# Kernel optimization log

Measured on AMD Instinct MI355X. Metric: run time of the kernel, lower is better.

## Reference

```python
import jax, jax.numpy as jnp
import numpy as np

C1 = 512  # channels1 (query input dim)
C = 512   # channels (model dim)


def setup_inputs() -> dict:
    key = jax.random.key(0)
    ks = jax.random.split(key, 12)
    B, Lq, Lk = 8, 2048, 2048
    s1 = 1.0 / np.sqrt(C1)
    s = 1.0 / np.sqrt(C)
    return {
        "rep": jax.random.normal(ks[0], (B, Lq, C1), dtype=jnp.float32),
        "rep1": jax.random.normal(ks[1], (B, Lk, C), dtype=jnp.float32),
        "Wq_w": jax.random.uniform(ks[2], (C1, C), jnp.float32, -s1, s1),
        "Wq_b": jax.random.uniform(ks[3], (C,), jnp.float32, -s1, s1),
        "Wk_w": jax.random.uniform(ks[4], (C, C), jnp.float32, -s, s),
        "Wk_b": jax.random.uniform(ks[5], (C,), jnp.float32, -s, s),
        "Wv_w": jax.random.uniform(ks[6], (C, C), jnp.float32, -s, s),
        "Wv_b": jax.random.uniform(ks[7], (C,), jnp.float32, -s, s),
        "FC_w": jax.random.uniform(ks[8], (C, C), jnp.float32, -s, s),
        "FC_b": jax.random.uniform(ks[9], (C,), jnp.float32, -s, s),
    }


def reference(rep, rep1, Wq_w, Wq_b, Wk_w, Wk_b, Wv_w, Wv_b, FC_w, FC_b):
    # Linear + ReLU projections (single head)
    q = jax.nn.relu(jnp.einsum('blc,cd->bld', rep, Wq_w) + Wq_b)    # [B,Lq,C]
    k = jax.nn.relu(jnp.einsum('blc,cd->bld', rep1, Wk_w) + Wk_b)   # [B,Lk,C]
    v = jax.nn.relu(jnp.einsum('blc,cd->bld', rep1, Wv_w) + Wv_b)   # [B,Lk,C]
    scores = jnp.einsum('bqd,bkd->bqk', q, k) / jnp.sqrt(jnp.float32(C))
    attn = jax.nn.softmax(scores, axis=-1)                           # [B,Lq,Lk]
    out = jnp.einsum('bqk,bkd->bqd', attn, v)                        # [B,Lq,C]
    out = jax.nn.relu(jnp.einsum('bld,de->ble', out, FC_w) + FC_b)
    return out
```

## Files before the change

kernel.cpp:

```cpp
#include <hip/hip_runtime.h>


typedef __attribute__((ext_vector_type(8))) short short8;
typedef __attribute__((ext_vector_type(4))) float f32x4;

#define SEQ 2048
#define CH 512
#define NB 8
#define MTOT (NB * SEQ)

#define GLDS16(gp, lp)                                                                  \
  __builtin_amdgcn_global_load_lds((const __attribute__((address_space(1))) void*)(gp), \
                                   (__attribute__((address_space(3))) void*)(lp), 16, 0, 0)

__device__ __forceinline__ unsigned short f2bf(float f) {
  unsigned u = __float_as_uint(f);
  u += 0x7fffu + ((u >> 16) & 1u);
  return (unsigned short)(u >> 16);
}

__global__ void cvt_bf16_kernel(const float* __restrict__ in0, unsigned short* __restrict__ out0,
                                const float* __restrict__ in1, unsigned short* __restrict__ out1) {
  int blk = blockIdx.x;
  const float* in = (blk < 4096) ? in0 : in1;
  unsigned short* out = (blk < 4096) ? out0 : out1;
  blk &= 4095;
  long i = ((long)blk * 256 + threadIdx.x) * 8;
  float4 a = *(const float4*)(in + i);
  float4 b = *(const float4*)(in + i + 4);
  ushort4 o0, o1;
  o0.x = f2bf(a.x); o0.y = f2bf(a.y); o0.z = f2bf(a.z); o0.w = f2bf(a.w);
  o1.x = f2bf(b.x); o1.y = f2bf(b.y); o1.z = f2bf(b.z); o1.w = f2bf(b.w);
  *(ushort4*)(out + i) = o0;
  *(ushort4*)(out + i + 4) = o1;
}

__global__ __launch_bounds__(256) void wtrans_kernel(const float* __restrict__ W0,
                                                     const float* __restrict__ W1,
                                                     const float* __restrict__ W2,
                                                     const float* __restrict__ W3,
                                                     unsigned short* __restrict__ Wt) {
  __shared__ __attribute__((aligned(16))) unsigned short tile[64 * 72];
  const int z = blockIdx.z;
  const float* W = (z == 0) ? W0 : (z == 1) ? W1 : (z == 2) ? W2 : W3;
  unsigned short* Wtz = Wt + (long)z * 512 * 512;
  const int t = threadIdx.x;
  const int k0 = blockIdx.y * 64, n0 = blockIdx.x * 64;
  const int r = t >> 4, cq = (t & 15) * 4;
#pragma unroll
  for (int j = 0; j < 4; ++j) {
    int row = r + 16 * j;
    float4 v = *(const float4*)&W[(long)(k0 + row) * 512 + n0 + cq];
    tile[row * 72 + cq + 0] = f2bf(v.x);
    tile[row * 72 + cq + 1] = f2bf(v.y);
    tile[row * 72 + cq + 2] = f2bf(v.z);
    tile[row * 72 + cq + 3] = f2bf(v.w);
  }
  __syncthreads();
#pragma unroll
  for (int j = 0; j < 4; ++j) {
    int row = r + 16 * j;
    ushort4 o;
    o.x = tile[(cq + 0) * 72 + row];
    o.y = tile[(cq + 1) * 72 + row];
    o.z = tile[(cq + 2) * 72 + row];
    o.w = tile[(cq + 3) * 72 + row];
    *(ushort4*)&Wtz[(long)(n0 + row) * 512 + k0 + cq] = o;
  }
}

__global__ __launch_bounds__(256) void vtrans_kernel(const unsigned short* __restrict__ V,
                                                     unsigned short* __restrict__ Vt) {
  __shared__ __attribute__((aligned(16))) unsigned short tile[64 * 72];
  const int t = threadIdx.x;
  const int b = blockIdx.z;
  const int kk0 = blockIdx.y * 64;
  const int d0 = blockIdx.x * 64;
  const unsigned short* Vb = V + (long)b * SEQ * CH;
  unsigned short* Vtb = Vt + (long)b * CH * SEQ;
  const int r = t >> 4, cq = (t & 15) * 4;
#pragma unroll
  for (int j = 0; j < 4; ++j) {
    int row = r + 16 * j;
    ushort4 v = *(const ushort4*)&Vb[(long)(kk0 + row) * CH + d0 + cq];
    tile[row * 72 + cq + 0] = v.x;
    tile[row * 72 + cq + 1] = v.y;
    tile[row * 72 + cq + 2] = v.z;
    tile[row * 72 + cq + 3] = v.w;
  }
  __syncthreads();
#pragma unroll
  for (int j = 0; j < 4; ++j) {
    int row = r + 16 * j;
    ushort4 o;
    o.x = tile[(cq + 0) * 72 + row];
    o.y = tile[(cq + 1) * 72 + row];
    o.z = tile[(cq + 2) * 72 + row];
    o.w = tile[(cq + 3) * 72 + row];
    *(ushort4*)&Vtb[(long)(d0 + row) * SEQ + kk0 + cq] = o;
  }
}

template <int EPI, int LDA, int LDB, int LDO, int K>
__global__ __launch_bounds__(256) void gemm_nt(const unsigned short* __restrict__ A, long sAb,
                                               const unsigned short* __restrict__ Bt, long sBb,
                                               const float* __restrict__ bias,
                                               float* __restrict__ rowsum, long sRb,
                                               void* __restrict__ outp, long sOb) {
  __shared__ __attribute__((aligned(16))) unsigned short Al[128 * 64];
  __shared__ __attribute__((aligned(16))) unsigned short Bl[128 * 64];
  const int t = threadIdx.x;
  const int w = t >> 6, l = t & 63;
  const int wr = w >> 1, wc = w & 1;
  const int lr = l & 15, lg = l >> 4;
  const int bz = blockIdx.z;
  const long m0 = (long)blockIdx.y * 128, n0 = (long)blockIdx.x * 128;
  const int srow = 32 * w + (l >> 3);
  const int sxor = ((l & 7) ^ (l >> 3)) * 8;
  const unsigned short* ga = A + bz * sAb + (long)(m0 + srow) * LDA + sxor;
  const unsigned short* gb = Bt + bz * sBb + (long)(n0 + srow) * LDB + sxor;
  unsigned short* la = &Al[32 * w * 64];
  unsigned short* lb = &Bl[32 * w * 64];

  f32x4 acc[4][4] = {};
  for (int k0 = 0; k0 < K; k0 += 64) {
#pragma unroll
    for (int j = 0; j < 4; ++j) {
      GLDS16(ga + (long)8 * j * LDA, la + j * 512);
      GLDS16(gb + (long)8 * j * LDB, lb + j * 512);
    }
    ga += 64; gb += 64;
    __syncthreads();
#pragma unroll
    for (int h = 0; h < 2; ++h) {
      short8 af[4], bfr[4];
#pragma unroll
      for (int i = 0; i < 4; ++i) {
        const int kc = ((h * 4 + lg) ^ (lr & 7)) * 8;
        af[i]  = *(short8*)&Al[(64 * wr + 16 * i + lr) * 64 + kc];
        bfr[i] = *(short8*)&Bl[(64 * wc + 16 * i + lr) * 64 + kc];
      }
#pragma unroll
      for (int mi = 0; mi < 4; ++mi)
#pragma unroll
        for (int ni = 0; ni < 4; ++ni)
          acc[mi][ni] =
              __builtin_amdgcn_mfma_f32_16x16x32_bf16(af[mi], bfr[ni], acc[mi][ni], 0, 0, 0);
    }
    __syncthreads();
  }

  if (EPI == 0) {
    float* patchF = (float*)(w < 2 ? Al : Bl) + (w & 1) * 1024;
    float* O = (float*)outp + bz * sOb;
    float bv[4];
#pragma unroll
    for (int ni = 0; ni < 4; ++ni) bv[ni] = bias[n0 + 64 * wc + 16 * ni + lr];
#pragma unroll
    for (int mi = 0; mi < 4; ++mi) {
      const long rowb = m0 + 64 * wr + 16 * mi;
#pragma unroll
      for (int ni = 0; ni < 4; ++ni)
#pragma unroll
        for (int r = 0; r < 4; ++r)
          patchF[(lg * 4 + r) * 64 + 16 * ni + lr] = fmaxf(acc[mi][ni][r] + bv[ni], 0.0f);
      __syncthreads();
#pragma unroll
      for (int j = 0; j < 4; ++j) {
        float4 x = *(float4*)&patchF[(4 * j + (l >> 4)) * 64 + (l & 15) * 4];
        *(float4*)&O[(rowb + 4 * j + (l >> 4)) * LDO + n0 + 64 * wc + (l & 15) * 4] = x;
      }
      __syncthreads();
    }
  } else {
    unsigned short* patch = &Al[w * 16 * 72];
    unsigned short* O = (unsigned short*)outp + bz * sOb;
    float bv[4];
    if (EPI == 1) {
#pragma unroll
      for (int ni = 0; ni < 4; ++ni) bv[ni] = bias[n0 + 64 * wc + 16 * ni + lr];
    }
    float rsum[4][4] = {};
    const float* rsin = (EPI == 3) ? rowsum + bz * sRb : nullptr;
#pragma unroll
    for (int mi = 0; mi < 4; ++mi) {
      const long rowb = m0 + 64 * wr + 16 * mi;
      float invr[4];
      if (EPI == 3) {
#pragma unroll
        for (int r = 0; r < 4; ++r) invr[r] = 1.0f / rsin[rowb + lg * 4 + r];
      }
#pragma unroll
      for (int ni = 0; ni < 4; ++ni)
#pragma unroll
        for (int r = 0; r < 4; ++r) {
          float a = acc[mi][ni][r];
          unsigned short ob;
          if (EPI == 1) {
            ob = f2bf(fmaxf(a + bv[ni], 0.0f));
          } else if (EPI == 2) {
            float p = exp2f(a * 0.06375872f);
            ob = f2bf(p);
            rsum[mi][r] += __uint_as_float((unsigned)ob << 16);
          } else {
            ob = f2bf(a * invr[r]);
          }
          patch[(lg * 4 + r) * 72 + 16 * ni + lr] = ob;
        }
      __syncthreads();
#pragma unroll
      for (int j = 0; j < 2; ++j) {
        short8 x = *(short8*)&patch[(l >> 2) * 72 + j * 32 + (l & 3) * 8];
        *(short8*)&O[(rowb + (l >> 2)) * LDO + n0 + 64 * wc + j * 32 + (l & 3) * 8] = x;
      }
      __syncthreads();
    }
    if (EPI == 2) {
      float* rs = rowsum + bz * sRb;
#pragma unroll
      for (int off = 1; off < 16; off <<= 1)
#pragma unroll
        for (int mi = 0; mi < 4; ++mi)
#pragma unroll
          for (int r = 0; r < 4; ++r) rsum[mi][r] += __shfl_xor(rsum[mi][r], off);
      if (lr == 0) {
#pragma unroll
        for (int mi = 0; mi < 4; ++mi)
#pragma unroll
          for (int r = 0; r < 4; ++r)
            atomicAdd(&rs[m0 + 64 * wr + 16 * mi + lg * 4 + r], rsum[mi][r]);
      }
    }
  }
}

extern "C" void kernel_launch(void* const* d_in, const int* in_sizes, int n_in,
                              void* d_out, int out_size, void* d_ws, size_t ws_size,
                              hipStream_t stream) {
  const float* rep  = (const float*)d_in[0];
  const float* rep1 = (const float*)d_in[1];
  const float* Wq_w = (const float*)d_in[2];
  const float* Wq_b = (const float*)d_in[3];
  const float* Wk_w = (const float*)d_in[4];
  const float* Wk_b = (const float*)d_in[5];
  const float* Wv_w = (const float*)d_in[6];
  const float* Wv_b = (const float*)d_in[7];
  const float* FC_w = (const float*)d_in[8];
  const float* FC_b = (const float*)d_in[9];
  float* out = (float*)d_out;
  char* ws = (char*)d_ws;

  const size_t SZB = (size_t)MTOT * CH * 2;
  const size_t SZP = (size_t)NB * SEQ * SEQ * 2;
  const size_t SZR = (size_t)MTOT * 4;
  const size_t need = 6 * SZB + 4 * (size_t)512 * 512 * 2 + SZP + SZR;
  if (ws_size < need) return;

  unsigned short* Qb    = (unsigned short*)(ws + 0 * SZB);
  unsigned short* Kbuf  = (unsigned short*)(ws + 1 * SZB);
  unsigned short* Vbuf  = (unsigned short*)(ws + 2 * SZB);
  unsigned short* Vtb   = (unsigned short*)(ws + 3 * SZB);
  unsigned short* repb  = (unsigned short*)(ws + 4 * SZB);
  unsigned short* rep1b = (unsigned short*)(ws + 5 * SZB);
  unsigned short* Wt4   = (unsigned short*)(ws + 6 * SZB);
  unsigned short* Wtq   = Wt4;
  unsigned short* Wtk   = Wtq + 512 * 512;
  unsigned short* Wtv   = Wtk + 512 * 512;
  unsigned short* Wtf   = Wtv + 512 * 512;
  unsigned short* Pbuf  = (unsigned short*)(ws + 6 * SZB + 4 * (size_t)512 * 512 * 2);
  float*          rowsum = (float*)((char*)Pbuf + SZP);

  hipMemsetAsync(rowsum, 0, SZR, stream);

  cvt_bf16_kernel<<<8192, 256, 0, stream>>>(rep, repb, rep1, rep1b);
  wtrans_kernel<<<dim3(8, 8, 4), 256, 0, stream>>>(Wq_w, Wk_w, Wv_w, FC_w, Wt4);

  gemm_nt<1, CH, CH, CH, CH><<<dim3(4, 128, 1), 256, 0, stream>>>(repb, 0, Wtq, 0, Wq_b,
                                                                  nullptr, 0, Qb, 0);
  gemm_nt<1, CH, CH, CH, CH><<<dim3(4, 128, 1), 256, 0, stream>>>(rep1b, 0, Wtk, 0, Wk_b,
                                                                  nullptr, 0, Kbuf, 0);
  gemm_nt<1, CH, CH, CH, CH><<<dim3(4, 128, 1), 256, 0, stream>>>(rep1b, 0, Wtv, 0, Wv_b,
                                                                  nullptr, 0, Vbuf, 0);

  vtrans_kernel<<<dim3(8, 32, 8), 256, 0, stream>>>(Vbuf, Vtb);

  gemm_nt<2, CH, CH, SEQ, CH><<<dim3(16, 16, 8), 256, 0, stream>>>(
      Qb, (long)SEQ * CH, Kbuf, (long)SEQ * CH, nullptr, rowsum, SEQ,
      Pbuf, (long)SEQ * SEQ);

  gemm_nt<3, SEQ, SEQ, CH, SEQ><<<dim3(4, 16, 8), 256, 0, stream>>>(
      Pbuf, (long)SEQ * SEQ, Vtb, (long)CH * SEQ, nullptr, rowsum, SEQ,
      Vbuf, (long)SEQ * CH);

  gemm_nt<0, CH, CH, CH, CH><<<dim3(4, 128, 1), 256, 0, stream>>>(Vbuf, 0, Wtf, 0, FC_b,
                                                                  nullptr, 0, out, 0);
}
```

Baseline: 317.7 us.

## Fold FC into V, fuse K/V projections, and use BK=128 tile for PV GEMM

Reassociates the FC projection so that V is multiplied by FC weights before attention, which lets the final PV GEMM apply the softmax normalisation, FC bias and ReLU directly. K and V projections become one GEMM writing interleaved KV with a concatenated bias. The PV GEMM uses a 128-wide K tile with a new swizzle, and the epilogues are reworked to stage the full 128x128 tile in LDS once. This removes one full-size GEMM launch and several intermediate buffers. The cost is an extra bf16 rounding of V·FC before attention.

```diff
diff --git a/kernel.cpp b/kernel.cpp
--- a/kernel.cpp
+++ b/kernel.cpp
@@ -101,44 +101,70 @@
   }
 }
 
-template <int EPI, int LDA, int LDB, int LDO, int K>
+template <int EPI, int LDA, int LDB, int LDO, int K, int BK>
 __global__ __launch_bounds__(256) void gemm_nt(const unsigned short* __restrict__ A, long sAb,
                                                const unsigned short* __restrict__ Bt, long sBb,
                                                const float* __restrict__ bias,
                                                float* __restrict__ rowsum, long sRb,
                                                void* __restrict__ outp, long sOb) {
-  __shared__ __attribute__((aligned(16))) unsigned short Al[128 * 64];
-  __shared__ __attribute__((aligned(16))) unsigned short Bl[128 * 64];
+  __shared__ __attribute__((aligned(16))) unsigned short smem[2 * 128 * BK];
+  unsigned short* Al = smem;
+  unsigned short* Bl = smem + 128 * BK;
   const int t = threadIdx.x;
   const int w = t >> 6, l = t & 63;
   const int wr = w >> 1, wc = w & 1;
   const int lr = l & 15, lg = l >> 4;
   const int bz = blockIdx.z;
   const long m0 = (long)blockIdx.y * 128, n0 = (long)blockIdx.x * 128;
-  const int srow = 32 * w + (l >> 3);
-  const int sxor = ((l & 7) ^ (l >> 3)) * 8;
-  const unsigned short* ga = A + bz * sAb + (long)(m0 + srow) * LDA + sxor;
-  const unsigned short* gb = Bt + bz * sBb + (long)(n0 + srow) * LDB + sxor;
-  unsigned short* la = &Al[32 * w * 64];
-  unsigned short* lb = &Bl[32 * w * 64];
+  const int NC = BK / 8;
+  const int rl = l / NC, cc0 = l % NC;
+  unsigned short* la = &Al[32 * w * BK];
+  unsigned short* lb = &Bl[32 * w * BK];
+  const unsigned short* gaJ[(BK == 128) ? 4 : 1];
+  const unsigned short* gbJ[(BK == 128) ? 4 : 1];
+  if (BK == 64) {
+    const int srow = 32 * w + rl;
+    const int sxor = (cc0 ^ (rl & 7)) * 8;
+    gaJ[0] = A + bz * sAb + (long)(m0 + srow) * LDA + sxor;
+    gbJ[0] = Bt + bz * sBb + (long)(n0 + srow) * LDB + sxor;
+  } else {
+#pragma unroll
+    for (int jm = 0; jm < 4; ++jm) {
+      const int srow = 32 * w + 4 * jm + rl;
+      const int sxor = (cc0 ^ ((4 * jm + rl) & 15)) * 8;
+      gaJ[jm] = A + bz * sAb + (long)(m0 + srow) * LDA + sxor;
+      gbJ[jm] = Bt + bz * sBb + (long)(n0 + srow) * LDB + sxor;
+    }
+  }
 
   f32x4 acc[4][4] = {};
-  for (int k0 = 0; k0 < K; k0 += 64) {
-#pragma unroll
-    for (int j = 0; j < 4; ++j) {
-      GLDS16(ga + (long)8 * j * LDA, la + j * 512);
-      GLDS16(gb + (long)8 * j * LDB, lb + j * 512);
-    }
-    ga += 64; gb += 64;
+  for (int k0 = 0; k0 < K; k0 += BK) {
+    if (BK == 64) {
+#pragma unroll
+      for (int j = 0; j < 4; ++j) {
+        GLDS16(gaJ[0] + (long)8 * j * LDA, la + j * 8 * 64);
+        GLDS16(gbJ[0] + (long)8 * j * LDB, lb + j * 8 * 64);
+      }
+      gaJ[0] += BK; gbJ[0] += BK;
+    } else {
+#pragma unroll
+      for (int jm = 0; jm < 4; ++jm) {
+        GLDS16(gaJ[jm], la + jm * 4 * 128);
+        GLDS16(gaJ[jm] + (long)16 * LDA, la + (16 + 4 * jm) * 128);
+        GLDS16(gbJ[jm], lb + jm * 4 * 128);
+        GLDS16(gbJ[jm] + (long)16 * LDB, lb + (16 + 4 * jm) * 128);
+        gaJ[jm] += BK; gbJ[jm] += BK;
+      }
+    }
     __syncthreads();
 #pragma unroll
-    for (int h = 0; h < 2; ++h) {
+    for (int h = 0; h < BK / 32; ++h) {
       short8 af[4], bfr[4];
 #pragma unroll
       for (int i = 0; i < 4; ++i) {
-        const int kc = ((h * 4 + lg) ^ (lr & 7)) * 8;
-        af[i]  = *(short8*)&Al[(64 * wr + 16 * i + lr) * 64 + kc];
-        bfr[i] = *(short8*)&Bl[(64 * wc + 16 * i + lr) * 64 + kc];
+        const int kc = ((h * 4 + lg) ^ (lr & (NC - 1))) * 8;
+        af[i]  = *(short8*)&Al[(64 * wr + 16 * i + lr) * BK + kc];
+        bfr[i] = *(short8*)&Bl[(64 * wc + 16 * i + lr) * BK + kc];
       }
 #pragma unroll
       for (int mi = 0; mi < 4; ++mi)
@@ -150,73 +176,48 @@
     __syncthreads();
   }
 
-  if (EPI == 0) {
-    float* patchF = (float*)(w < 2 ? Al : Bl) + (w & 1) * 1024;
-    float* O = (float*)outp + bz * sOb;
-    float bv[4];
-#pragma unroll
-    for (int ni = 0; ni < 4; ++ni) bv[ni] = bias[n0 + 64 * wc + 16 * ni + lr];
-#pragma unroll
-    for (int mi = 0; mi < 4; ++mi) {
-      const long rowb = m0 + 64 * wr + 16 * mi;
-#pragma unroll
-      for (int ni = 0; ni < 4; ++ni)
-#pragma unroll
-        for (int r = 0; r < 4; ++r)
-          patchF[(lg * 4 + r) * 64 + 16 * ni + lr] = fmaxf(acc[mi][ni][r] + bv[ni], 0.0f);
-      __syncthreads();
-#pragma unroll
-      for (int j = 0; j < 4; ++j) {
-        float4 x = *(float4*)&patchF[(4 * j + (l >> 4)) * 64 + (l & 15) * 4];
-        *(float4*)&O[(rowb + 4 * j + (l >> 4)) * LDO + n0 + 64 * wc + (l & 15) * 4] = x;
-      }
-      __syncthreads();
-    }
-  } else {
-    unsigned short* patch = &Al[w * 16 * 72];
-    unsigned short* O = (unsigned short*)outp + bz * sOb;
+  if (EPI == 1 || EPI == 6 || EPI == 2) {
+    unsigned short* patch = smem;
     float bv[4];
     if (EPI == 1) {
 #pragma unroll
       for (int ni = 0; ni < 4; ++ni) bv[ni] = bias[n0 + 64 * wc + 16 * ni + lr];
     }
     float rsum[4][4] = {};
-    const float* rsin = (EPI == 3) ? rowsum + bz * sRb : nullptr;
-#pragma unroll
-    for (int mi = 0; mi < 4; ++mi) {
-      const long rowb = m0 + 64 * wr + 16 * mi;
-      float invr[4];
-      if (EPI == 3) {
-#pragma unroll
-        for (int r = 0; r < 4; ++r) invr[r] = 1.0f / rsin[rowb + lg * 4 + r];
-      }
+#pragma unroll
+    for (int mi = 0; mi < 4; ++mi)
 #pragma unroll
       for (int ni = 0; ni < 4; ++ni)
 #pragma unroll
         for (int r = 0; r < 4; ++r) {
+          const int m = 64 * wr + 16 * mi + 4 * lg + r;
+          const int n = 64 * wc + 16 * ni + lr;
           float a = acc[mi][ni][r];
           unsigned short ob;
-          if (EPI == 1) {
-            ob = f2bf(fmaxf(a + bv[ni], 0.0f));
-          } else if (EPI == 2) {
+          if (EPI == 1)      ob = f2bf(fmaxf(a + bv[ni], 0.0f));
+          else if (EPI == 6) ob = f2bf(a);
+          else {
             float p = exp2f(a * 0.06375872f);
             ob = f2bf(p);
             rsum[mi][r] += __uint_as_float((unsigned)ob << 16);
-          } else {
-            ob = f2bf(a * invr[r]);
           }
-          patch[(lg * 4 + r) * 72 + 16 * ni + lr] = ob;
+          patch[m * 128 + ((n >> 3) ^ (m & 15)) * 8 + (n & 7)] = ob;
         }
-      __syncthreads();
-#pragma unroll
-      for (int j = 0; j < 2; ++j) {
-        short8 x = *(short8*)&patch[(l >> 2) * 72 + j * 32 + (l & 3) * 8];
-        *(short8*)&O[(rowb + (l >> 2)) * LDO + n0 + 64 * wc + j * 32 + (l & 3) * 8] = x;
-      }
-      __syncthreads();
+    __syncthreads();
+    unsigned short* O = (unsigned short*)outp + bz * sOb;
+    const int q = t & 3;
+#pragma unroll
+    for (int p = 0; p < 2; ++p) {
+      const int m = 64 * p + (t >> 2);
+#pragma unroll
+      for (int i = 0; i < 4; ++i) {
+        const int cc = i * 4 + q;
+        short8 x = *(short8*)&patch[m * 128 + ((cc ^ (m & 15)) * 8)];
+        *(short8*)&O[(m0 + m) * LDO + n0 + cc * 8] = x;
+      }
     }
     if (EPI == 2) {
-      float* rs = rowsum + bz * sRb;
+      float* rsw = rowsum + bz * sRb;
 #pragma unroll
       for (int off = 1; off < 16; off <<= 1)
 #pragma unroll
@@ -228,7 +229,43 @@
         for (int mi = 0; mi < 4; ++mi)
 #pragma unroll
           for (int r = 0; r < 4; ++r)
-            atomicAdd(&rs[m0 + 64 * wr + 16 * mi + lg * 4 + r], rsum[mi][r]);
+            atomicAdd(&rsw[m0 + 64 * wr + 16 * mi + 4 * lg + r], rsum[mi][r]);
+      }
+    }
+  } else {
+    float* patchF = (float*)smem;
+    float bv[4];
+#pragma unroll
+    for (int ni = 0; ni < 4; ++ni) bv[ni] = bias[n0 + 64 * wc + 16 * ni + lr];
+    const float* rs = rowsum + bz * sRb;
+    float inv[4][4];
+#pragma unroll
+    for (int mi = 0; mi < 4; ++mi)
+#pragma unroll
+      for (int r = 0; r < 4; ++r)
+        inv[mi][r] = 1.0f / rs[m0 + 64 * wr + 16 * mi + 4 * lg + r];
+#pragma unroll
+    for (int mi = 0; mi < 4; ++mi)
+#pragma unroll
+      for (int ni = 0; ni < 4; ++ni)
+#pragma unroll
+        for (int r = 0; r < 4; ++r) {
+          const int m = 64 * wr + 16 * mi + 4 * lg + r;
+          const int n = 64 * wc + 16 * ni + lr;
+          patchF[m * 128 + ((n >> 2) ^ (m & 31)) * 4 + (n & 3)] =
+              fmaxf(acc[mi][ni][r] * inv[mi][r] + bv[ni], 0.0f);
+        }
+    __syncthreads();
+    float* O = (float*)outp + bz * sOb;
+    const int q = t & 3;
+#pragma unroll
+    for (int p = 0; p < 2; ++p) {
+      const int m = 64 * p + (t >> 2);
+#pragma unroll
+      for (int i = 0; i < 8; ++i) {
+        const int cc = i * 4 + q;
+        f32x4 x = *(f32x4*)&patchF[m * 128 + ((cc ^ (m & 31)) * 4)];
+        *(f32x4*)&O[(m0 + m) * LDO + n0 + cc * 4] = x;
       }
     }
   }
@@ -250,48 +287,46 @@
   float* out = (float*)d_out;
   char* ws = (char*)d_ws;
 
-  const size_t SZB = (size_t)MTOT * CH * 2;
-  const size_t SZP = (size_t)NB * SEQ * SEQ * 2;
-  const size_t SZR = (size_t)MTOT * 4;
-  const size_t need = 6 * SZB + 4 * (size_t)512 * 512 * 2 + SZP + SZR;
+  const size_t MB = 1024 * 1024;
+  unsigned short* Qb     = (unsigned short*)(ws + 0 * MB);
+  unsigned short* KVb    = (unsigned short*)(ws + 16 * MB);
+  unsigned short* repb   = (unsigned short*)(ws + 48 * MB);
+  unsigned short* rep1b  = (unsigned short*)(ws + 64 * MB);
+  unsigned short* Wt4    = (unsigned short*)(ws + 80 * MB);
+  float*          biasKV = (float*)(ws + 82 * MB);
+  unsigned short* Pbuf   = (unsigned short*)(ws + 83 * MB);
+  float*          rowsum = (float*)(ws + 147 * MB);
+  const size_t need = 148 * MB;
   if (ws_size < need) return;
 
-  unsigned short* Qb    = (unsigned short*)(ws + 0 * SZB);
-  unsigned short* Kbuf  = (unsigned short*)(ws + 1 * SZB);
-  unsigned short* Vbuf  = (unsigned short*)(ws + 2 * SZB);
-  unsigned short* Vtb   = (unsigned short*)(ws + 3 * SZB);
-  unsigned short* repb  = (unsigned short*)(ws + 4 * SZB);
-  unsigned short* rep1b = (unsigned short*)(ws + 5 * SZB);
-  unsigned short* Wt4   = (unsigned short*)(ws + 6 * SZB);
-  unsigned short* Wtq   = Wt4;
-  unsigned short* Wtk   = Wtq + 512 * 512;
-  unsigned short* Wtv   = Wtk + 512 * 512;
-  unsigned short* Wtf   = Wtv + 512 * 512;
-  unsigned short* Pbuf  = (unsigned short*)(ws + 6 * SZB + 4 * (size_t)512 * 512 * 2);
-  float*          rowsum = (float*)((char*)Pbuf + SZP);
-
-  hipMemsetAsync(rowsum, 0, SZR, stream);
+  unsigned short* WtQ = Wt4;
+  unsigned short* WtKV = Wt4 + 512 * 512;
+  unsigned short* WtF = Wt4 + 3 * 512 * 512;
+  unsigned short* VFn = repb;
+  unsigned short* VFt = rep1b;
+
+  hipMemsetAsync(rowsum, 0, MTOT * 4, stream);
+  hipMemcpyAsync(biasKV, Wk_b, 512 * 4, hipMemcpyDeviceToDevice, stream);
+  hipMemcpyAsync(biasKV + 512, Wv_b, 512 * 4, hipMemcpyDeviceToDevice, stream);
 
   cvt_bf16_kernel<<<8192, 256, 0, stream>>>(rep, repb, rep1, rep1b);
   wtrans_kernel<<<dim3(8, 8, 4), 256, 0, stream>>>(Wq_w, Wk_w, Wv_w, FC_w, Wt4);
 
-  gemm_nt<1, CH, CH, CH, CH><<<dim3(4, 128, 1), 256, 0, stream>>>(repb, 0, Wtq, 0, Wq_b,
-                                                                  nullptr, 0, Qb, 0);
-  gemm_nt<1, CH, CH, CH, CH><<<dim3(4, 128, 1), 256, 0, stream>>>(rep1b, 0, Wtk, 0, Wk_b,
-                                                                  nullptr, 0, Kbuf, 0);
-  gemm_nt<1, CH, CH, CH, CH><<<dim3(4, 128, 1), 256, 0, stream>>>(rep1b, 0, Wtv, 0, Wv_b,
-                                                                  nullptr, 0, Vbuf, 0);
-
-  vtrans_kernel<<<dim3(8, 32, 8), 256, 0, stream>>>(Vbuf, Vtb);
-
-  gemm_nt<2, CH, CH, SEQ, CH><<<dim3(16, 16, 8), 256, 0, stream>>>(
-      Qb, (long)SEQ * CH, Kbuf, (long)SEQ * CH, nullptr, rowsum, SEQ,
+  gemm_nt<1, CH, CH, CH, CH, 64><<<dim3(4, 128, 1), 256, 0, stream>>>(
+      repb, 0, WtQ, 0, Wq_b, nullptr, 0, Qb, 0);
+  gemm_nt<1, CH, CH, 1024, CH, 64><<<dim3(8, 128, 1), 256, 0, stream>>>(
+      rep1b, 0, WtKV, 0, biasKV, nullptr, 0, KVb, 0);
+
+  gemm_nt<6, 1024, CH, CH, CH, 64><<<dim3(4, 16, 8), 256, 0, stream>>>(
+      KVb + 512, (long)SEQ * 1024, WtF, 0, nullptr, nullptr, 0, VFn, (long)SEQ * CH);
+
+  vtrans_kernel<<<dim3(8, 32, 8), 256, 0, stream>>>(VFn, VFt);
+
+  gemm_nt<2, CH, 1024, SEQ, CH, 64><<<dim3(16, 16, 8), 256, 0, stream>>>(
+      Qb, (long)SEQ * CH, KVb, (long)SEQ * 1024, nullptr, rowsum, SEQ,
       Pbuf, (long)SEQ * SEQ);
 
-  gemm_nt<3, SEQ, SEQ, CH, SEQ><<<dim3(4, 16, 8), 256, 0, stream>>>(
-      Pbuf, (long)SEQ * SEQ, Vtb, (long)CH * SEQ, nullptr, rowsum, SEQ,
-      Vbuf, (long)SEQ * CH);
-
-  gemm_nt<0, CH, CH, CH, CH><<<dim3(4, 128, 1), 256, 0, stream>>>(Vbuf, 0, Wtf, 0, FC_b,
-                                                                  nullptr, 0, out, 0);
-}
+  gemm_nt<5, SEQ, SEQ, CH, SEQ, 128><<<dim3(4, 16, 8), 256, 0, stream>>>(
+      Pbuf, (long)SEQ * SEQ, VFt, (long)CH * SEQ, FC_b, rowsum, SEQ,
+      (void*)out, (long)SEQ * CH);
+}
```

Result: slower. 326.2 us (+2.7%).
